# Kernel tuning notes

Hardware: AMD Instinct MI355X
Metric: run time of the kernel (lower is better)

The kernel has to match this reference:

```python
import jax, jax.numpy as jnp
import numpy as np

NUM_LAYERS = 32
IN_SIZE = 1024
OUT_SIZE = 1024
B, S = 32, 256


def setup_inputs() -> dict:
    key = jax.random.key(0)
    k1, k2, k3 = jax.random.split(key, 3)
    x = jax.random.normal(k1, (B, S, IN_SIZE), dtype=jnp.float32)
    layer_idx = jax.random.randint(k2, (S,), 0, NUM_LAYERS, dtype=jnp.int32)
    # learned parameter: per-layer weight [L, O, D], normal(stddev=1.0) as in flax init
    weight = jax.random.normal(k3, (NUM_LAYERS, OUT_SIZE, IN_SIZE), dtype=jnp.float32)
    return {"x": x, "layer_idx": layer_idx, "weight": weight}


def reference(x, layer_idx, weight):
    # x: [B, S, D]; layer_idx: [S]; weight: [L, O, D]
    # Each sequence position s uses expert weight[layer_idx[s]]:
    #   out[b, s, o] = sum_d x[b, s, d] * weight[layer_idx[s], o, d]
    w = weight[layer_idx]                      # [S, O, D] gather
    return jnp.einsum('bsd,sod->bso', x, w)    # [B, S, O]
```

## Files before the change

kernel.cpp:

```cpp
#include <hip/hip_runtime.h>
#include <hip/hip_bf16.h>
#include <stdint.h>

#define NLAYERS 32
#define DSIZE   1024
#define OSIZE   1024
#define BATCH   32
#define SEQ     256

#define WS_PERM  16
#define WS_TILE  512
#define MAX_TILES 88

typedef __attribute__((ext_vector_type(8)))  short short8;
typedef __attribute__((ext_vector_type(16))) float f32x16;

#define LDSTRIDE 72
#define BK 64
#define NSPLIT 16

__global__ void prep_kernel(const int* __restrict__ layer_idx, int* __restrict__ wsi) {
    __shared__ int cnt[NLAYERS];
    __shared__ int start_[NLAYERS];
    __shared__ int cursor[NLAYERS];
    const int t = threadIdx.x;
    if (t < NLAYERS) cnt[t] = 0;
    __syncthreads();
    int l = 0;
    if (t < SEQ) { l = layer_idx[t]; atomicAdd(&cnt[l], 1); }
    __syncthreads();
    if (t == 0) {
        int acc = 0;
        for (int i = 0; i < NLAYERS; ++i) { start_[i] = acc; cursor[i] = acc; acc += cnt[i]; }
    }
    __syncthreads();
    if (t < SEQ) {
        int r = atomicAdd(&cursor[l], 1);
        wsi[WS_PERM + r] = t;
    }
    if (t == 0) {
        int nt = 0;
        for (int i = 0; i < NLAYERS; ++i) {
            const int c = cnt[i];
            for (int j = 0; j < c; j += 4) {
                wsi[WS_TILE + nt*4 + 0] = i;
                wsi[WS_TILE + nt*4 + 1] = start_[i] + j;
                wsi[WS_TILE + nt*4 + 2] = (c - j < 4) ? (c - j) : 4;
                ++nt;
            }
        }
        wsi[0] = nt;
    }
}

static __device__ __forceinline__ unsigned pk2(float a, float b) {
    unsigned ua = __builtin_bit_cast(unsigned, a) + 0x8000u;
    unsigned ub = __builtin_bit_cast(unsigned, b) + 0x8000u;
    return __builtin_amdgcn_perm(ub, ua, 0x07060302u);
}

__global__ __launch_bounds__(256, 3) void gemm_kernel(
        const float* __restrict__ x, const float* __restrict__ wgt,
        const int* __restrict__ wsi, float* __restrict__ out) {
    const int ntiles = wsi[0];
    const int mt = blockIdx.y;
    if (mt >= ntiles) return;
    const int layer     = wsi[WS_TILE + mt*4 + 0];
    const int rank_base = wsi[WS_TILE + mt*4 + 1];
    const int nranks    = wsi[WS_TILE + mt*4 + 2];
    const int ntile     = blockIdx.x;

    __shared__ __align__(16) short ldsA[128 * LDSTRIDE];
    __shared__ __align__(16) short ldsB[64 * LDSTRIDE];

    const int t     = threadIdx.x;
    const int c4    = (t & 15) * 4;
    const int rbase = t >> 4;

    bool svalid[4];
    int  sv[4];
    #pragma unroll
    for (int j = 0; j < 4; ++j) {
        svalid[j] = (j < nranks);
        sv[j] = svalid[j] ? wsi[WS_PERM + rank_base + j] : 0;
    }

    const float* aptr[8];
    #pragma unroll
    for (int p = 0; p < 8; ++p) {
        const int roff = p >> 1;
        const int b    = rbase + ((p & 1) << 4);
        aptr[p] = x + (((size_t)(b * SEQ + sv[roff])) << 10) + c4;
    }
    const float* bbase = wgt + (((size_t)((layer << 10) + ntile * 64 + rbase)) << 10) + c4;

    float4 ra[8], rb[4];
    auto load_step = [&](int kk) {
        #pragma unroll
        for (int p = 0; p < 8; ++p) {
            if (svalid[p >> 1]) ra[p] = *(const float4*)(aptr[p] + kk);
            else                ra[p] = make_float4(0.f, 0.f, 0.f, 0.f);
        }
        #pragma unroll
        for (int p = 0; p < 4; ++p)
            rb[p] = *(const float4*)(bbase + ((size_t)p << 14) + kk);
    };

    const int lane = t & 63;
    const int wv   = t >> 6;
    const int wm   = wv * 32;
    const int l31  = lane & 31;
    const int lh   = lane >> 5;

    f32x16 acc[2];
    #pragma unroll
    for (int ni = 0; ni < 2; ++ni)
        #pragma unroll
        for (int r = 0; r < 16; ++r) acc[ni][r] = 0.f;

    const short* pA0 = &ldsA[(wm + l31) * LDSTRIDE + lh * 8];
    const short* pB0 = &ldsB[l31 * LDSTRIDE + lh * 8];

    load_step(0);
    #pragma unroll 1
    for (int kk = 0; kk < DSIZE; kk += BK) {
        __syncthreads();
        #pragma unroll
        for (int p = 0; p < 8; ++p) {
            const int row = rbase + 16 * p;
            uint2 va;
            va.x = pk2(ra[p].x, ra[p].y);
            va.y = pk2(ra[p].z, ra[p].w);
            *(uint2*)&ldsA[row * LDSTRIDE + c4] = va;
        }
        #pragma unroll
        for (int p = 0; p < 4; ++p) {
            const int row = rbase + 16 * p;
            uint2 vb;
            vb.x = pk2(rb[p].x, rb[p].y);
            vb.y = pk2(rb[p].z, rb[p].w);
            *(uint2*)&ldsB[row * LDSTRIDE + c4] = vb;
        }
        __syncthreads();
        if (kk + BK < DSIZE) load_step(kk + BK);
        #pragma unroll
        for (int sub = 0; sub < 4; ++sub) {
            short8 a0 = *(const short8*)(pA0 + sub*16);
            short8 b0 = *(const short8*)(pB0 + sub*16);
            short8 b1 = *(const short8*)(pB0 + 32*LDSTRIDE + sub*16);
            acc[0] = __builtin_amdgcn_mfma_f32_32x32x16_bf16(a0, b0, acc[0], 0, 0, 0);
            acc[1] = __builtin_amdgcn_mfma_f32_32x32x16_bf16(a0, b1, acc[1], 0, 0, 0);
        }
    }

    if (wv < nranks) {
        const int s = wsi[WS_PERM + rank_base + wv];
        #pragma unroll
        for (int ni = 0; ni < 2; ++ni) {
            const int ocol = ntile * 64 + ni * 32 + l31;
            #pragma unroll
            for (int r = 0; r < 16; ++r) {
                const int brow = (r & 3) + 8 * (r >> 2) + 4 * lh;
                out[(((size_t)(brow * SEQ + s)) << 10) + ocol] = acc[ni][r];
            }
        }
    }
}

extern "C" void kernel_launch(void* const* d_in, const int* in_sizes, int n_in,
                              void* d_out, int out_size, void* d_ws, size_t ws_size,
                              hipStream_t stream) {
    const float* x         = (const float*)d_in[0];
    const int*   layer_idx = (const int*)  d_in[1];
    const float* weight    = (const float*)d_in[2];
    float* out = (float*)d_out;
    int*   wsi = (int*)d_ws;

    prep_kernel<<<1, 256, 0, stream>>>(layer_idx, wsi);
    gemm_kernel<<<dim3(NSPLIT, MAX_TILES), 256, 0, stream>>>(x, weight, wsi, out);
}
```

Before: 251.5 us.

## Enlarge GEMM tiles to 256x256 with 8-position chunks and swizzled LDS

The grouping step now packs sequence positions into chunks of up to 8 per layer instead of 4. Each 512-thread block computes a 256x256 output tile: 8 positions times 32 batch rows, by 256 output columns. Each wave holds a 2x4 grid of 32x32 MFMA accumulators, and LDS rows are XOR-swizzled instead of padded. The aim is to cut how often each expert weight row is re-streamed and converted, and to raise MFMA work per LDS load. In exchange the grid shrinks to 256 blocks with a fixed chunk-to-block mapping, so partially filled chunks waste work and occupancy is lower.

Result: slower. 260.2 us (+3.5%).

```diff
diff --git a/kernel.cpp b/kernel.cpp
--- a/kernel.cpp
+++ b/kernel.cpp
@@ -1,5 +1,4 @@
 #include <hip/hip_runtime.h>
-#include <hip/hip_bf16.h>
 #include <stdint.h>
 
 #define NLAYERS 32
@@ -10,14 +9,16 @@
 
 #define WS_PERM  16
 #define WS_TILE  512
-#define MAX_TILES 88
+#define CHUNK    8
+#define MAXC     60
+#define BK       64
+#define TM       256
+#define TN       256
+#define THREADS  512
 
 typedef __attribute__((ext_vector_type(8)))  short short8;
 typedef __attribute__((ext_vector_type(16))) float f32x16;
-
-#define LDSTRIDE 72
-#define BK 64
-#define NSPLIT 16
+typedef __attribute__((ext_vector_type(4)))  unsigned uint4v;
 
 __global__ void prep_kernel(const int* __restrict__ layer_idx, int* __restrict__ wsi) {
     __shared__ int cnt[NLAYERS];
@@ -39,17 +40,17 @@
         wsi[WS_PERM + r] = t;
     }
     if (t == 0) {
-        int nt = 0;
+        int nc = 0;
         for (int i = 0; i < NLAYERS; ++i) {
             const int c = cnt[i];
-            for (int j = 0; j < c; j += 4) {
-                wsi[WS_TILE + nt*4 + 0] = i;
-                wsi[WS_TILE + nt*4 + 1] = start_[i] + j;
-                wsi[WS_TILE + nt*4 + 2] = (c - j < 4) ? (c - j) : 4;
-                ++nt;
-            }
-        }
-        wsi[0] = nt;
+            for (int j = 0; j < c; j += CHUNK) {
+                wsi[WS_TILE + nc*4 + 0] = i;
+                wsi[WS_TILE + nc*4 + 1] = start_[i] + j;
+                wsi[WS_TILE + nc*4 + 2] = (c - j < CHUNK) ? (c - j) : CHUNK;
+                ++nc;
+            }
+        }
+        wsi[0] = nc;
     }
 }
 
@@ -59,109 +60,145 @@
     return __builtin_amdgcn_perm(ub, ua, 0x07060302u);
 }
 
-__global__ __launch_bounds__(256, 3) void gemm_kernel(
+__global__ __launch_bounds__(THREADS, 2) void gemm_kernel(
         const float* __restrict__ x, const float* __restrict__ wgt,
         const int* __restrict__ wsi, float* __restrict__ out) {
-    const int ntiles = wsi[0];
-    const int mt = blockIdx.y;
-    if (mt >= ntiles) return;
-    const int layer     = wsi[WS_TILE + mt*4 + 0];
-    const int rank_base = wsi[WS_TILE + mt*4 + 1];
-    const int nranks    = wsi[WS_TILE + mt*4 + 2];
-    const int ntile     = blockIdx.x;
-
-    __shared__ __align__(16) short ldsA[128 * LDSTRIDE];
-    __shared__ __align__(16) short ldsB[64 * LDSTRIDE];
-
-    const int t     = threadIdx.x;
-    const int c4    = (t & 15) * 4;
-    const int rbase = t >> 4;
-
-    bool svalid[4];
-    int  sv[4];
-    #pragma unroll
-    for (int j = 0; j < 4; ++j) {
-        svalid[j] = (j < nranks);
-        sv[j] = svalid[j] ? wsi[WS_PERM + rank_base + j] : 0;
-    }
-
-    const float* aptr[8];
-    #pragma unroll
-    for (int p = 0; p < 8; ++p) {
-        const int roff = p >> 1;
-        const int b    = rbase + ((p & 1) << 4);
-        aptr[p] = x + (((size_t)(b * SEQ + sv[roff])) << 10) + c4;
-    }
-    const float* bbase = wgt + (((size_t)((layer << 10) + ntile * 64 + rbase)) << 10) + c4;
-
-    float4 ra[8], rb[4];
+    const int fid = blockIdx.x;
+    const int g     = (fid & 7) | ((fid >> 5) << 3);
+    const int ntile = (fid >> 3) & 3;
+    const int nchunks = wsi[0];
+    if (g >= nchunks) return;
+    const int layer     = wsi[WS_TILE + g*4 + 0];
+    const int rank_base = wsi[WS_TILE + g*4 + 1];
+    const int nranks    = wsi[WS_TILE + g*4 + 2];
+
+    __shared__ __align__(16) short ldsA[TM * BK];
+    __shared__ __align__(16) short ldsB[TN * BK];
+
+    const int t    = threadIdx.x;
+    const int slot = t & 7;
+    const int rb   = t >> 3;
+    const int wsw  = ((slot ^ (rb & 7)) << 3);
+
+    const float* aptr[4];
+    bool av[4];
+    #pragma unroll
+    for (int p = 0; p < 4; ++p) {
+        const int r  = rb + 64*p;
+        const int ro = r >> 5;
+        const int b  = r & 31;
+        av[p] = (ro < nranks);
+        const int s = av[p] ? wsi[WS_PERM + rank_base + ro] : 0;
+        aptr[p] = x + (((size_t)(b * SEQ + s)) << 10) + slot*8;
+    }
+    const float* bptr = wgt + ((size_t)layer << 20)
+                            + (((size_t)(ntile * TN + rb)) << 10) + slot*8;
+
+    float4 ra[4][2], rbv[4][2];
     auto load_step = [&](int kk) {
         #pragma unroll
-        for (int p = 0; p < 8; ++p) {
-            if (svalid[p >> 1]) ra[p] = *(const float4*)(aptr[p] + kk);
-            else                ra[p] = make_float4(0.f, 0.f, 0.f, 0.f);
-        }
-        #pragma unroll
-        for (int p = 0; p < 4; ++p)
-            rb[p] = *(const float4*)(bbase + ((size_t)p << 14) + kk);
+        for (int p = 0; p < 4; ++p) {
+            if (av[p]) {
+                ra[p][0] = *(const float4*)(aptr[p] + kk);
+                ra[p][1] = *(const float4*)(aptr[p] + kk + 4);
+            }
+        }
+        #pragma unroll
+        for (int p = 0; p < 4; ++p) {
+            rbv[p][0] = *(const float4*)(bptr + ((size_t)p << 16) + kk);
+            rbv[p][1] = *(const float4*)(bptr + ((size_t)p << 16) + kk + 4);
+        }
     };
 
     const int lane = t & 63;
     const int wv   = t >> 6;
-    const int wm   = wv * 32;
     const int l31  = lane & 31;
     const int lh   = lane >> 5;
-
-    f32x16 acc[2];
-    #pragma unroll
-    for (int ni = 0; ni < 2; ++ni)
-        #pragma unroll
-        for (int r = 0; r < 16; ++r) acc[ni][r] = 0.f;
-
-    const short* pA0 = &ldsA[(wm + l31) * LDSTRIDE + lh * 8];
-    const short* pB0 = &ldsB[l31 * LDSTRIDE + lh * 8];
+    const int wm   = (wv >> 1) * 64;
+    const int wn   = (wv & 1) * 128;
+    const int rsw  = l31 & 7;
+
+    const int baseA0 = (wm +  0 + l31) * BK;
+    const int baseA1 = (wm + 32 + l31) * BK;
+    int baseB[4];
+    #pragma unroll
+    for (int ni = 0; ni < 4; ++ni) baseB[ni] = (wn + ni*32 + l31) * BK;
+
+    const int rank0 = wm >> 5;
+    const bool ok0 = (rank0 + 0) < nranks;
+    const bool ok1 = (rank0 + 1) < nranks;
+
+    f32x16 acc[2][4];
+    #pragma unroll
+    for (int mi = 0; mi < 2; ++mi)
+        #pragma unroll
+        for (int ni = 0; ni < 4; ++ni)
+            #pragma unroll
+            for (int r = 0; r < 16; ++r) acc[mi][ni][r] = 0.f;
 
     load_step(0);
     #pragma unroll 1
     for (int kk = 0; kk < DSIZE; kk += BK) {
         __syncthreads();
         #pragma unroll
-        for (int p = 0; p < 8; ++p) {
-            const int row = rbase + 16 * p;
-            uint2 va;
-            va.x = pk2(ra[p].x, ra[p].y);
-            va.y = pk2(ra[p].z, ra[p].w);
-            *(uint2*)&ldsA[row * LDSTRIDE + c4] = va;
-        }
-        #pragma unroll
-        for (int p = 0; p < 4; ++p) {
-            const int row = rbase + 16 * p;
-            uint2 vb;
-            vb.x = pk2(rb[p].x, rb[p].y);
-            vb.y = pk2(rb[p].z, rb[p].w);
-            *(uint2*)&ldsB[row * LDSTRIDE + c4] = vb;
+        for (int p = 0; p < 4; ++p) {
+            if (av[p]) {
+                uint4v u;
+                u.x = pk2(ra[p][0].x, ra[p][0].y);
+                u.y = pk2(ra[p][0].z, ra[p][0].w);
+                u.z = pk2(ra[p][1].x, ra[p][1].y);
+                u.w = pk2(ra[p][1].z, ra[p][1].w);
+                *(uint4v*)&ldsA[(rb + 64*p) * BK + wsw] = u;
+            }
+        }
+        #pragma unroll
+        for (int p = 0; p < 4; ++p) {
+            uint4v u;
+            u.x = pk2(rbv[p][0].x, rbv[p][0].y);
+            u.y = pk2(rbv[p][0].z, rbv[p][0].w);
+            u.z = pk2(rbv[p][1].x, rbv[p][1].y);
+            u.w = pk2(rbv[p][1].z, rbv[p][1].w);
+            *(uint4v*)&ldsB[(rb + 64*p) * BK + wsw] = u;
         }
         __syncthreads();
         if (kk + BK < DSIZE) load_step(kk + BK);
-        #pragma unroll
-        for (int sub = 0; sub < 4; ++sub) {
-            short8 a0 = *(const short8*)(pA0 + sub*16);
-            short8 b0 = *(const short8*)(pB0 + sub*16);
-            short8 b1 = *(const short8*)(pB0 + 32*LDSTRIDE + sub*16);
-            acc[0] = __builtin_amdgcn_mfma_f32_32x32x16_bf16(a0, b0, acc[0], 0, 0, 0);
-            acc[1] = __builtin_amdgcn_mfma_f32_32x32x16_bf16(a0, b1, acc[1], 0, 0, 0);
-        }
-    }
-
-    if (wv < nranks) {
-        const int s = wsi[WS_PERM + rank_base + wv];
-        #pragma unroll
-        for (int ni = 0; ni < 2; ++ni) {
-            const int ocol = ntile * 64 + ni * 32 + l31;
+        if (ok0) {
             #pragma unroll
-            for (int r = 0; r < 16; ++r) {
-                const int brow = (r & 3) + 8 * (r >> 2) + 4 * lh;
-                out[(((size_t)(brow * SEQ + s)) << 10) + ocol] = acc[ni][r];
+            for (int sub = 0; sub < 4; ++sub) {
+                const int gx = (((sub*2 + lh) ^ rsw) << 3);
+                short8 b0[4];
+                #pragma unroll
+                for (int ni = 0; ni < 4; ++ni)
+                    b0[ni] = *(const short8*)&ldsB[baseB[ni] + gx];
+                {
+                    short8 a0 = *(const short8*)&ldsA[baseA0 + gx];
+                    #pragma unroll
+                    for (int ni = 0; ni < 4; ++ni)
+                        acc[0][ni] = __builtin_amdgcn_mfma_f32_32x32x16_bf16(a0, b0[ni], acc[0][ni], 0, 0, 0);
+                }
+                if (ok1) {
+                    short8 a1 = *(const short8*)&ldsA[baseA1 + gx];
+                    #pragma unroll
+                    for (int ni = 0; ni < 4; ++ni)
+                        acc[1][ni] = __builtin_amdgcn_mfma_f32_32x32x16_bf16(a1, b0[ni], acc[1][ni], 0, 0, 0);
+                }
+            }
+        }
+    }
+
+    #pragma unroll
+    for (int mi = 0; mi < 2; ++mi) {
+        const int ro = rank0 + mi;
+        if (ro < nranks) {
+            const int s = wsi[WS_PERM + rank_base + ro];
+            #pragma unroll
+            for (int ni = 0; ni < 4; ++ni) {
+                const int ocol = ntile * TN + wn + ni*32 + l31;
+                #pragma unroll
+                for (int r = 0; r < 16; ++r) {
+                    const int brow = (r & 3) + 8*(r >> 2) + 4*lh;
+                    out[(((size_t)(brow * SEQ + s)) << 10) + ocol] = acc[mi][ni][r];
+                }
             }
         }
     }
@@ -177,5 +214,5 @@
     int*   wsi = (int*)d_ws;
 
     prep_kernel<<<1, 256, 0, stream>>>(layer_idx, wsi);
-    gemm_kernel<<<dim3(NSPLIT, MAX_TILES), 256, 0, stream>>>(x, weight, wsi, out);
-}
+    gemm_kernel<<<256, THREADS, 0, stream>>>(x, weight, wsi, out);
+}
```
